# Performance work log

Measured on AMD Instinct MI355X. Metric: run time of the kernel, lower is better.

Reference implementation:

```python
import jax, jax.numpy as jnp
import numpy as np

B, L, D = 64, 1024, 1280

def setup_inputs() -> dict:
    key = jax.random.key(0)
    k1, k2, k3, k4, k5, k6 = jax.random.split(key, 6)
    prev_result = jax.random.normal(k1, (B, L, D), dtype=jnp.float32)
    lengths = jax.random.randint(k2, (B,), 0, 1022)
    dense_w = jax.random.normal(k3, (D, D), dtype=jnp.float32) * 0.02
    dense_b = jax.random.normal(k4, (D,), dtype=jnp.float32) * 0.02
    cls_w = jax.random.normal(k5, (D, 1), dtype=jnp.float32) * 0.02
    cls_b = jax.random.normal(k6, (1,), dtype=jnp.float32) * 0.02
    return {"prev_result": prev_result, "lengths": lengths,
            "dense_w": dense_w, "dense_b": dense_b,
            "cls_w": cls_w, "cls_b": cls_b}

def reference(prev_result, lengths, dense_w, dense_b, cls_w, cls_b):
    # ragged mean pool over first (len + 2) tokens of each sequence
    pool_len = lengths + 2                                  # [B]
    mask = (jnp.arange(L)[None, :] < pool_len[:, None])     # [B, L]
    mask_f = mask.astype(prev_result.dtype)
    summed = jnp.einsum('bld,bl->bd', prev_result, mask_f)  # [B, D]
    embedding = summed / pool_len[:, None].astype(prev_result.dtype)
    x = jax.nn.relu(embedding @ dense_w + dense_b)          # [B, D]
    return x @ cls_w + cls_b                                # [B, 1]
```

## Files before the change

### kernel.cpp

```cpp
#include <hip/hip_runtime.h>

#define BB 64
#define LL 1024
#define DD 1280
#define SPLITS 8
#define CHUNK 128
#define NCOL 5

__global__ __launch_bounds__(320) void pool_partial(
    const float* __restrict__ prev, const int* __restrict__ lengths,
    float* __restrict__ P) {
  const int s = blockIdx.x;
  const int b = blockIdx.y;
  const int t = threadIdx.x;

  const int pool_len = lengths[b] + 2;
  const int l0 = s * CHUNK;
  const int l1 = min(pool_len, l0 + CHUNK);

  float4 acc = make_float4(0.f, 0.f, 0.f, 0.f);
  const float* base = prev + (size_t)b * LL * DD + 4 * t;
#pragma unroll 4
  for (int l = l0; l < l1; ++l) {
    const float4 v = *(const float4*)(base + (size_t)l * DD);
    acc.x += v.x; acc.y += v.y; acc.z += v.z; acc.w += v.w;
  }
  float4* dst = (float4*)(P + ((size_t)s * BB + b) * DD) + t;
  *dst = acc;
}

__global__ __launch_bounds__(256) void gemm_relu_partial(
    const float* __restrict__ P, const int* __restrict__ lengths,
    const float* __restrict__ W, const float* __restrict__ bias,
    const float* __restrict__ cls_w, float* __restrict__ Q) {
  __shared__ float emb[DD];
  __shared__ float red[4];

  const int c = blockIdx.x;
  const int b = blockIdx.y;
  const int t = threadIdx.x;

  const float inv = 1.0f / (float)(lengths[b] + 2);
  for (int d = t; d < DD; d += 256) {
    float s = 0.f;
#pragma unroll
    for (int k = 0; k < SPLITS; ++k) s += P[((size_t)k * BB + b) * DD + d];
    emb[d] = s * inv;
  }
  __syncthreads();

  const int col = c * 256 + t;
  float acc = bias[col];
#pragma unroll 8
  for (int d = 0; d < DD; ++d) {
    acc = fmaf(emb[d], W[(size_t)d * DD + col], acc);
  }
  float v = fmaxf(acc, 0.f) * cls_w[col];

#pragma unroll
  for (int off = 32; off > 0; off >>= 1) v += __shfl_down(v, off);
  const int lane = t & 63;
  const int wave = t >> 6;
  if (lane == 0) red[wave] = v;
  __syncthreads();
  if (t == 0) Q[b * NCOL + c] = red[0] + red[1] + red[2] + red[3];
}

__global__ __launch_bounds__(64) void final_out(
    const float* __restrict__ Q, const float* __restrict__ cls_b,
    float* __restrict__ out) {
  const int b = threadIdx.x;
  if (b < BB) {
    float s = cls_b[0];
#pragma unroll
    for (int c = 0; c < NCOL; ++c) s += Q[b * NCOL + c];
    out[b] = s;
  }
}

extern "C" void kernel_launch(void* const* d_in, const int* in_sizes, int n_in,
                              void* d_out, int out_size, void* d_ws, size_t ws_size,
                              hipStream_t stream) {
  const float* prev    = (const float*)d_in[0];
  const int*   lengths = (const int*)d_in[1];
  const float* dense_w = (const float*)d_in[2];
  const float* dense_b = (const float*)d_in[3];
  const float* cls_w   = (const float*)d_in[4];
  const float* cls_b   = (const float*)d_in[5];
  float* out = (float*)d_out;

  float* P = (float*)d_ws;
  float* Q = P + (size_t)SPLITS * BB * DD;

  pool_partial<<<dim3(SPLITS, BB), 320, 0, stream>>>(prev, lengths, P);
  gemm_relu_partial<<<dim3(NCOL, BB), 256, 0, stream>>>(P, lengths, dense_w,
                                                        dense_b, cls_w, Q);
  final_out<<<1, 64, 0, stream>>>(Q, cls_b, out);
}
```

Before: 498.9 us.

## Split pooling finer and reuse dense weights across four batch rows

```diff
diff --git a/kernel.cpp b/kernel.cpp
--- a/kernel.cpp
+++ b/kernel.cpp
@@ -3,9 +3,10 @@
 #define BB 64
 #define LL 1024
 #define DD 1280
-#define SPLITS 8
-#define CHUNK 128
-#define NCOL 5
+#define SPLITS 16
+#define CHUNK 64
+#define CC 20
+#define BG 16
 
 __global__ __launch_bounds__(320) void pool_partial(
     const float* __restrict__ prev, const int* __restrict__ lengths,
@@ -29,53 +30,55 @@
   *dst = acc;
 }
 
-__global__ __launch_bounds__(256) void gemm_relu_partial(
+__global__ __launch_bounds__(320) void emb_reduce(
     const float* __restrict__ P, const int* __restrict__ lengths,
-    const float* __restrict__ W, const float* __restrict__ bias,
-    const float* __restrict__ cls_w, float* __restrict__ Q) {
-  __shared__ float emb[DD];
-  __shared__ float red[4];
-
-  const int c = blockIdx.x;
-  const int b = blockIdx.y;
+    const float* __restrict__ cls_b, float* __restrict__ emb,
+    float* __restrict__ out) {
+  const int b = blockIdx.x;
   const int t = threadIdx.x;
 
   const float inv = 1.0f / (float)(lengths[b] + 2);
-  for (int d = t; d < DD; d += 256) {
-    float s = 0.f;
+  float4 acc = make_float4(0.f, 0.f, 0.f, 0.f);
 #pragma unroll
-    for (int k = 0; k < SPLITS; ++k) s += P[((size_t)k * BB + b) * DD + d];
-    emb[d] = s * inv;
+  for (int s = 0; s < SPLITS; ++s) {
+    const float4 v = *((const float4*)(P + ((size_t)s * BB + b) * DD) + t);
+    acc.x += v.x; acc.y += v.y; acc.z += v.z; acc.w += v.w;
   }
+  acc.x *= inv; acc.y *= inv; acc.z *= inv; acc.w *= inv;
+  *((float4*)(emb + (size_t)b * DD) + t) = acc;
+  if (t == 0) out[b] = cls_b[0];
+}
+
+__global__ __launch_bounds__(256) void gemm_relu_out(
+    const float* __restrict__ emb, const float* __restrict__ W,
+    const float* __restrict__ bias, const float* __restrict__ cls_w,
+    float* __restrict__ out) {
+  __shared__ float es[4 * DD];
+
+  const int cc = blockIdx.x;
+  const int bg = blockIdx.y;
+  const int t = threadIdx.x;
+  const int lane = t & 63;
+  const int wave = t >> 6;
+  const int b = bg * 4 + wave;
+  const int col = cc * 64 + lane;
+
+  const float* eg = emb + (size_t)bg * 4 * DD;
+  for (int i = t; i < 4 * DD; i += 256) es[i] = eg[i];
   __syncthreads();
 
-  const int col = c * 256 + t;
+  const float* ew = es + wave * DD;
+  const float* wp = W + col;
   float acc = bias[col];
-#pragma unroll 8
+#pragma unroll 16
   for (int d = 0; d < DD; ++d) {
-    acc = fmaf(emb[d], W[(size_t)d * DD + col], acc);
+    acc = fmaf(ew[d], wp[(size_t)d * DD], acc);
   }
   float v = fmaxf(acc, 0.f) * cls_w[col];
 
 #pragma unroll
   for (int off = 32; off > 0; off >>= 1) v += __shfl_down(v, off);
-  const int lane = t & 63;
-  const int wave = t >> 6;
-  if (lane == 0) red[wave] = v;
-  __syncthreads();
-  if (t == 0) Q[b * NCOL + c] = red[0] + red[1] + red[2] + red[3];
-}
-
-__global__ __launch_bounds__(64) void final_out(
-    const float* __restrict__ Q, const float* __restrict__ cls_b,
-    float* __restrict__ out) {
-  const int b = threadIdx.x;
-  if (b < BB) {
-    float s = cls_b[0];
-#pragma unroll
-    for (int c = 0; c < NCOL; ++c) s += Q[b * NCOL + c];
-    out[b] = s;
-  }
+  if (lane == 0) atomicAdd(out + b, v);
 }
 
 extern "C" void kernel_launch(void* const* d_in, const int* in_sizes, int n_in,
@@ -90,10 +93,10 @@
   float* out = (float*)d_out;
 
   float* P = (float*)d_ws;
-  float* Q = P + (size_t)SPLITS * BB * DD;
+  float* emb = P + (size_t)SPLITS * BB * DD;
 
   pool_partial<<<dim3(SPLITS, BB), 320, 0, stream>>>(prev, lengths, P);
-  gemm_relu_partial<<<dim3(NCOL, BB), 256, 0, stream>>>(P, lengths, dense_w,
-                                                        dense_b, cls_w, Q);
-  final_out<<<1, 64, 0, stream>>>(Q, cls_b, out);
+  emb_reduce<<<BB, 320, 0, stream>>>(P, lengths, cls_b, emb, out);
+  gemm_relu_out<<<dim3(CC, BG), 256, 0, stream>>>(emb, dense_w, dense_b,
+                                                  cls_w, out);
 }
```

Measured after the change: 474.4 us. 4.9% less time.
